# Kernel optimization log

Measured on AMD Instinct MI355X. Metric: run time of the kernel, lower is better.

## Reference

```python
import jax, jax.numpy as jnp
import numpy as np

EMBED_DIM = 512
NUM_HEADS = 8
HEAD_DIM = EMBED_DIM // NUM_HEADS
B, N, M = 4, 4096, 4096


def setup_inputs() -> dict:
    key = jax.random.key(0)
    ks = jax.random.split(key, 16)
    s = 0.02
    inp = {
        "query": jax.random.normal(ks[0], (B, N, EMBED_DIM), jnp.float32),
        "key": jax.random.normal(ks[1], (B, M, EMBED_DIM), jnp.float32),
        "value": jax.random.normal(ks[2], (B, M, EMBED_DIM), jnp.float32),
        # Linear weights stored as (in, out) so y = x @ W + b (== torch x @ W.T + b)
        "Wq": jax.random.normal(ks[3], (EMBED_DIM, EMBED_DIM), jnp.float32) * s,
        "bq": jnp.zeros((EMBED_DIM,), jnp.float32),
        "Wk": jax.random.normal(ks[4], (EMBED_DIM, EMBED_DIM), jnp.float32) * s,
        "bk": jnp.zeros((EMBED_DIM,), jnp.float32),
        "Wv": jax.random.normal(ks[5], (EMBED_DIM, EMBED_DIM), jnp.float32) * s,
        "bv": jnp.zeros((EMBED_DIM,), jnp.float32),
        # rank expansion MLP acts per-head on head_dim
        "W1": jax.random.normal(ks[6], (HEAD_DIM, HEAD_DIM * 2), jnp.float32) * s,
        "b1": jnp.zeros((HEAD_DIM * 2,), jnp.float32),
        "W2": jax.random.normal(ks[7], (HEAD_DIM * 2, HEAD_DIM), jnp.float32) * s,
        "b2": jnp.zeros((HEAD_DIM,), jnp.float32),
        "Wo": jax.random.normal(ks[8], (EMBED_DIM, EMBED_DIM), jnp.float32) * s,
        "bo": jnp.zeros((EMBED_DIM,), jnp.float32),
    }
    return inp


def reference(query, key, value, Wq, bq, Wk, bk, Wv, bv, W1, b1, W2, b2, Wo, bo):
    b, n, _ = query.shape
    m = key.shape[1]
    H, D = NUM_HEADS, HEAD_DIM
    # ELU+1 feature maps on projected q, k
    q = jax.nn.elu(query @ Wq + bq) + 1.0           # [B,N,E]
    k = jax.nn.elu(key @ Wk + bk) + 1.0             # [B,M,E]
    v = value @ Wv + bv                              # [B,M,E]
    q = q.reshape(b, n, H, D)
    k = k.reshape(b, m, H, D)
    v = v.reshape(b, m, H, D)
    # rank expansion MLP on keys (per head_dim), exact GELU as nn.GELU default
    k_aug = jax.nn.gelu(k @ W1 + b1, approximate=False) @ W2 + b2
    k_aug = jax.nn.elu(k_aug) + 1.0                  # [B,M,H,D]
    # inputs already fp32 (torch .float() casts are identity here)
    k_scaled = k_aug / m                             # normalize over context len
    kv_context = jnp.einsum('bmhd,bmhe->bhde', k_scaled, v)   # [B,H,D,D]
    out = jnp.einsum('bnhd,bhde->bnhe', q, kv_context)        # [B,N,H,D]
    k_sum = k_scaled.sum(axis=1)                      # [B,H,D]
    denom = jnp.einsum('bnhd,bhd->bnh', q, k_sum)     # [B,N,H]
    out = out / jnp.clip(denom, 1e-6, None)[..., None]
    out = jnp.clip(jnp.nan_to_num(out, nan=0.0, posinf=65000.0, neginf=-65000.0),
                   -65000.0, 65000.0)
    out = out.reshape(b, n, H * D)
    return out @ Wo + bo
```

## Files before the change

kernel.cpp:

```cpp
#include <hip/hip_runtime.h>
#include <hip/hip_bf16.h>
#include <cmath>

#define DEV __device__ __forceinline__

typedef __bf16 bf16x8 __attribute__((ext_vector_type(8)));
typedef float f32x4 __attribute__((ext_vector_type(4)));
typedef unsigned int u32;
typedef unsigned short u16;

#define S_VMCNT(N) asm volatile("s_waitcnt vmcnt(" #N ")" ::: "memory")
#define S_LGKM0    asm volatile("s_waitcnt lgkmcnt(0)" ::: "memory")
#define S_FENCE    asm volatile("" ::: "memory")
#define S_BAR      __builtin_amdgcn_s_barrier()

DEV u16 f2bf(float f) {
  union { float f; u32 u; } v;
  v.f = f;
  u32 u = v.u;
  u += 0x7fffu + ((u >> 16) & 1u);
  return (u16)(u >> 16);
}
DEV u32 pk2(float a, float b) {
  union { __hip_bfloat162 h2; u32 u; } v;
  v.h2 = __float22bfloat162_rn(float2{a, b});
  return v.u;
}

DEV void async16(const void* g, void* l) {
  __builtin_amdgcn_global_load_lds((const __attribute__((address_space(1))) u32*)g,
                                   (__attribute__((address_space(3))) u32*)l, 16, 0, 0);
}

DEV int swz(int row, int kq) { return row * 64 + ((kq * 8) ^ ((row & 7) << 3)); }

__global__ __launch_bounds__(256, 2)
void qkv_gemm(const float* __restrict__ qin, const float* __restrict__ kin,
              const float* __restrict__ vin, const u16* __restrict__ WqP,
              const u16* __restrict__ WkP, const u16* __restrict__ WvP,
              const float* __restrict__ bq, const float* __restrict__ bk,
              const float* __restrict__ bv, u16* __restrict__ qact,
              u16* __restrict__ kact, u16* __restrict__ vT)
{
  __shared__ __align__(16) u16 SB[32768];

  const int z = blockIdx.z;
  const float* Af = z == 0 ? qin : z == 1 ? kin : vin;
  const u16* Bp = z == 0 ? WqP : z == 1 ? WkP : WvP;
  const float* bias = z == 0 ? bq : z == 1 ? bk : bv;

  const int tid = threadIdx.x, wv = tid >> 6, lane = tid & 63;
  const int wr = wv >> 1, wc = wv & 1;
  const int lrow = lane & 15, lq = lane >> 4;
  const long r0 = (long)blockIdx.x * 128;
  const int c0 = blockIdx.y * 128;

  f32x4 acc[4][4] = {};
  float4 rA[2][8];

  auto loadA = [&](float4* dst, int T) {
#pragma unroll
    for (int it = 0; it < 4; ++it) {
      const int s = it * 256 + tid;
      const int row = s >> 3, kq = s & 7;
      const float* g = Af + (r0 + row) * 512 + T * 64 + kq * 8;
      dst[2 * it]     = *(const float4*)g;
      dst[2 * it + 1] = *(const float4*)(g + 4);
    }
  };
  auto cvtStoreA = [&](const float4* src, u16* bufA) {
#pragma unroll
    for (int it = 0; it < 4; ++it) {
      const int s = it * 256 + tid;
      const int row = s >> 3, kq = s & 7;
      union { u32 q[4]; uint4 v; } pk;
      pk.q[0] = pk2(src[2 * it].x, src[2 * it].y);
      pk.q[1] = pk2(src[2 * it].z, src[2 * it].w);
      pk.q[2] = pk2(src[2 * it + 1].x, src[2 * it + 1].y);
      pk.q[3] = pk2(src[2 * it + 1].z, src[2 * it + 1].w);
      *(uint4*)&bufA[swz(row, kq)] = pk.v;
    }
  };
  auto issueB = [&](int T, u16* bufB) {
#pragma unroll
    for (int it = 0; it < 4; ++it) {
      const int sl = it * 256 + wv * 64;
      async16(Bp + ((long)blockIdx.y * 8 + T) * 8192 + (sl + lane) * 8, &bufB[sl * 8]);
    }
  };
  auto computeT = [&](const u16* Ac, const u16* Bc) {
#pragma unroll
    for (int subk = 0; subk < 2; ++subk) {
      bf16x8 af[4], bfr[4];
#pragma unroll
      for (int i = 0; i < 4; ++i)
        af[i] = *(const bf16x8*)&Ac[swz(wr * 64 + i * 16 + lrow, subk * 4 + lq)];
#pragma unroll
      for (int j = 0; j < 4; ++j)
        bfr[j] = *(const bf16x8*)&Bc[swz(wc * 64 + j * 16 + lrow, subk * 4 + lq)];
#pragma unroll
      for (int i = 0; i < 4; ++i)
#pragma unroll
        for (int j = 0; j < 4; ++j)
          acc[i][j] = __builtin_amdgcn_mfma_f32_16x16x32_bf16(af[i], bfr[j], acc[i][j], 0, 0, 0);
    }
  };

  issueB(0, SB + 8192);
  S_FENCE;
  loadA(rA[0], 0);
  loadA(rA[1], 1);
  cvtStoreA(rA[0], SB);
  S_LGKM0;
  S_VMCNT(8);
  S_BAR;

#pragma unroll
  for (int t = 0; t < 8; ++t) {
    const int cur = t & 1, nxt = 1 - cur;
    u16* Ac = SB + cur * 16384;
    u16* Bc = Ac + 8192;
    u16* An = SB + nxt * 16384;
    u16* Bn = An + 8192;
    if (t < 7) issueB(t + 1, Bn);
    S_FENCE;
    if (t < 6) loadA(rA[cur], t + 2);
    if (t < 7) cvtStoreA(rA[nxt], An);
    computeT(Ac, Bc);
    S_LGKM0;
    if (t < 6)       { S_VMCNT(8); }
    else if (t == 6) { S_VMCNT(0); }
    S_BAR;
  }

  if (z < 2) {
    u16* Y = z == 0 ? qact : kact;
#pragma unroll
    for (int i = 0; i < 4; ++i) {
#pragma unroll
      for (int j = 0; j < 4; ++j) {
        const int col = c0 + wc * 64 + j * 16 + lrow;
        const float bvv = bias[col];
#pragma unroll
        for (int p = 0; p < 4; ++p) {
          float o = acc[i][j][p] + bvv;
          o = (o > 0.f) ? (o + 1.f) : __expf(o);
          const long row = r0 + wr * 64 + i * 16 + lq * 4 + p;
          Y[row * 512 + col] = f2bf(o);
        }
      }
    }
  } else {
    u16* LTv = SB + wv * 4608;
#pragma unroll
    for (int i = 0; i < 4; ++i) {
#pragma unroll
      for (int j = 0; j < 4; ++j) {
        const int col = c0 + wc * 64 + j * 16 + lrow;
        const float bvv = bias[col];
        ushort4 w;
        w.x = f2bf(acc[i][j][0] + bvv);
        w.y = f2bf(acc[i][j][1] + bvv);
        w.z = f2bf(acc[i][j][2] + bvv);
        w.w = f2bf(acc[i][j][3] + bvv);
        *(ushort4*)&LTv[(j * 16 + lrow) * 72 + i * 16 + lq * 4] = w;
      }
    }
    const int b = (int)(r0 >> 12);
    const int h = (c0 + wc * 64) >> 6;
    const int mg0 = (int)(r0 & 4095) + wr * 64;
#pragma unroll
    for (int ps = 0; ps < 8; ++ps) {
      const int e = ps * 8 + (lane >> 3);
      const int mq = (lane & 7) * 8;
      uint4 v = *(const uint4*)&LTv[e * 72 + mq];
      *(uint4*)(vT + (((long)b * 8 + h) * 64 + e) * 4096 + mg0 + mq) = v;
    }
  }
}

__global__ __launch_bounds__(256, 2)
void out_gemm(const u16* __restrict__ A, const u16* __restrict__ Bt,
              const float* __restrict__ bias, float* __restrict__ Y)
{
  __shared__ __align__(16) u16 SB[32768];
  const int tid = threadIdx.x, wv = tid >> 6, lane = tid & 63;
  const int wr = wv >> 1, wc = wv & 1;
  const int lrow = lane & 15, lq = lane >> 4;
  const long r0 = (long)blockIdx.x * 128;
  const int c0 = blockIdx.y * 128;

  auto stage = [&](int T, u16* buf) {
#pragma unroll
    for (int it = 0; it < 4; ++it) {
      const int sl = it * 256 + wv * 64;
      async16(A  + ((long)blockIdx.x * 8 + T) * 8192 + (sl + lane) * 8, &buf[sl * 8]);
      async16(Bt + ((long)blockIdx.y * 8 + T) * 8192 + (sl + lane) * 8, &buf[8192 + sl * 8]);
    }
  };

  f32x4 acc[4][4] = {};
  stage(0, SB);
  S_VMCNT(0);
  S_BAR;

#pragma unroll
  for (int t = 0; t < 8; ++t) {
    const int cur = t & 1, nxt = 1 - cur;
    if (t < 7) stage(t + 1, SB + nxt * 16384);
    const u16* Ac = SB + cur * 16384;
    const u16* Bc = Ac + 8192;
#pragma unroll
    for (int subk = 0; subk < 2; ++subk) {
      bf16x8 af[4], bfr[4];
#pragma unroll
      for (int i = 0; i < 4; ++i)
        af[i] = *(const bf16x8*)&Ac[swz(wr * 64 + i * 16 + lrow, subk * 4 + lq)];
#pragma unroll
      for (int j = 0; j < 4; ++j)
        bfr[j] = *(const bf16x8*)&Bc[swz(wc * 64 + j * 16 + lrow, subk * 4 + lq)];
#pragma unroll
      for (int i = 0; i < 4; ++i)
#pragma unroll
        for (int j = 0; j < 4; ++j)
          acc[i][j] = __builtin_amdgcn_mfma_f32_16x16x32_bf16(af[i], bfr[j], acc[i][j], 0, 0, 0);
    }
    S_LGKM0;
    if (t < 7) { S_VMCNT(0); }
    S_BAR;
  }
#pragma unroll
  for (int i = 0; i < 4; ++i) {
#pragma unroll
    for (int j = 0; j < 4; ++j) {
      const int col = c0 + wc * 64 + j * 16 + lrow;
      const float bv = bias[col];
#pragma unroll
      for (int p = 0; p < 4; ++p) {
        const long row = r0 + wr * 64 + i * 16 + lq * 4 + p;
        Y[row * 512 + col] = acc[i][j][p] + bv;
      }
    }
  }
}

struct TArgs {
  const float* src[6];
  u16* dst[6];
  int K[6];
  int N[6];
};
__global__ __launch_bounds__(256)
void transpose_w(TArgs a)
{
  const int m = blockIdx.z;
  const int K = a.K[m], N = a.N[m];
  const int kt = blockIdx.y * 64, nt = blockIdx.x * 64;
  if (kt >= K || nt >= N) return;
  const float* src = a.src[m];
  u16* dst = a.dst[m];
  __shared__ u16 t[64][72];
  const int tx = threadIdx.x & 15, ty = threadIdx.x >> 4;
#pragma unroll
  for (int rr = 0; rr < 64; rr += 16) {
    const int k = kt + ty + rr;
    float4 v = *(const float4*)(src + (long)k * N + nt + tx * 4);
    t[tx * 4 + 0][ty + rr] = f2bf(v.x);
    t[tx * 4 + 1][ty + rr] = f2bf(v.y);
    t[tx * 4 + 2][ty + rr] = f2bf(v.z);
    t[tx * 4 + 3][ty + rr] = f2bf(v.w);
  }
  __syncthreads();
  if (m < 4) {
    const int ktile = kt >> 6;
#pragma unroll
    for (int it = 0; it < 2; ++it) {
      const int s = threadIdx.x + it * 256;
      const int r = s >> 3, c = (s & 7) * 8;
      const int n = nt + r;
      const int colblk = n >> 7, cl = n & 127;
      ushort4 u0 = *(ushort4*)&t[r][c];
      ushort4 u1 = *(ushort4*)&t[r][c + 4];
      u16* d = dst + ((long)colblk * 8 + ktile) * 8192 + cl * 64 + (c ^ ((cl & 7) << 3));
      *(ushort4*)d = u0;
      *(ushort4*)(d + 4) = u1;
    }
  } else {
#pragma unroll
    for (int it = 0; it < 2; ++it) {
      const int s = threadIdx.x + it * 256;
      const int r = s >> 3, c = (s & 7) * 8;
      ushort4 u0 = *(ushort4*)&t[r][c];
      ushort4 u1 = *(ushort4*)&t[r][c + 4];
      *(ushort4*)(dst + (long)(nt + r) * K + kt + c) = u0;
      *(ushort4*)(dst + (long)(nt + r) * K + kt + c + 4) = u1;
    }
  }
}

__global__ __launch_bounds__(256)
void mlp_fused(const u16* __restrict__ kact, const u16* __restrict__ W1T,
               const u16* __restrict__ W2T, const float* __restrict__ b1,
               const float* __restrict__ b2, u16* __restrict__ kaT, float invM)
{
  __shared__ __align__(16) u16 SB[27136];
  u16* As  = SB;
  u16* W1p = SB + 9216;
  u16* W2p = SB + 18432;
  u16* hid = SB;
  u16* LT2 = SB;

  const int tid = threadIdx.x, wv = tid >> 6, lane = tid & 63;
  const int lrow = lane & 15, lq = lane >> 4;
  const int bh = blockIdx.y, b = bh >> 3, h = bh & 7;
  const int m0 = blockIdx.x * 128;
  const long kbase = ((long)b * 4096 + m0) * 512 + h * 64;

#pragma unroll
  for (int i = 0; i < 4; ++i) {
    const int c = i * 256 + tid;
    const int row = c >> 3, p = c & 7;
    uint4 v = *(const uint4*)(kact + kbase + (long)row * 512 + p * 8);
    *(uint4*)&As[row * 72 + p * 8] = v;
  }
#pragma unroll
  for (int i = 0; i < 4; ++i) {
    const int c = i * 256 + tid;
    const int row = c >> 3, p = c & 7;
    uint4 v = *(const uint4*)(W1T + c * 8);
    *(uint4*)&W1p[row * 72 + p * 8] = v;
  }
#pragma unroll
  for (int i = 0; i < 4; ++i) {
    const int c = i * 256 + tid;
    const int row = c >> 4, p = c & 15;
    uint4 v = *(const uint4*)(W2T + c * 8);
    *(uint4*)&W2p[row * 136 + p * 8] = v;
  }
  __syncthreads();

  const int c0 = (wv >> 1) * 64, mh0 = (wv & 1) * 64;
  f32x4 acc1[4][4] = {};
#pragma unroll
  for (int kt = 0; kt < 2; ++kt) {
    bf16x8 wa[4], kb[4];
#pragma unroll
    for (int i = 0; i < 4; ++i)
      wa[i] = *(const bf16x8*)&W1p[(c0 + i * 16 + lrow) * 72 + kt * 32 + lq * 8];
#pragma unroll
    for (int j = 0; j < 4; ++j)
      kb[j] = *(const bf16x8*)&As[(mh0 + j * 16 + lrow) * 72 + kt * 32 + lq * 8];
#pragma unroll
    for (int i = 0; i < 4; ++i)
#pragma unroll
      for (int j = 0; j < 4; ++j)
        acc1[i][j] = __builtin_amdgcn_mfma_f32_16x16x32_bf16(wa[i], kb[j], acc1[i][j], 0, 0, 0);
  }
  __syncthreads();

#pragma unroll
  for (int i = 0; i < 4; ++i) {
    const int cc = c0 + i * 16 + lq * 4;
    float4 bv = *(const float4*)(b1 + cc);
#pragma unroll
    for (int j = 0; j < 4; ++j) {
      const int m = mh0 + j * 16 + lrow;
      float x0 = acc1[i][j][0] + bv.x, x1 = acc1[i][j][1] + bv.y;
      float x2 = acc1[i][j][2] + bv.z, x3 = acc1[i][j][3] + bv.w;
      ushort4 w;
      w.x = f2bf(0.5f * x0 * (1.f + erff(x0 * 0.7071067811865475f)));
      w.y = f2bf(0.5f * x1 * (1.f + erff(x1 * 0.7071067811865475f)));
      w.z = f2bf(0.5f * x2 * (1.f + erff(x2 * 0.7071067811865475f)));
      w.w = f2bf(0.5f * x3 * (1.f + erff(x3 * 0.7071067811865475f)));
      *(ushort4*)&hid[m * 136 + cc] = w;
    }
  }
  __syncthreads();

  const int d0 = (wv >> 1) * 32, mh2 = (wv & 1) * 64;
  f32x4 acc2[4][2] = {};
#pragma unroll
  for (int kt = 0; kt < 4; ++kt) {
    bf16x8 wa[2], hb[4];
#pragma unroll
    for (int i = 0; i < 2; ++i)
      wa[i] = *(const bf16x8*)&W2p[(d0 + i * 16 + lrow) * 136 + kt * 32 + lq * 8];
#pragma unroll
    for (int j = 0; j < 4; ++j)
      hb[j] = *(const bf16x8*)&hid[(mh2 + j * 16 + lrow) * 136 + kt * 32 + lq * 8];
#pragma unroll
    for (int j = 0; j < 4; ++j)
#pragma unroll
      for (int i = 0; i < 2; ++i)
        acc2[j][i] = __builtin_amdgcn_mfma_f32_16x16x32_bf16(hb[j], wa[i], acc2[j][i], 0, 0, 0);
  }
  __syncthreads();

#pragma unroll
  for (int i = 0; i < 2; ++i) {
    const int d = d0 + i * 16 + lrow;
    const float bd = b2[d];
#pragma unroll
    for (int j = 0; j < 4; ++j) {
      const int ml = mh2 + j * 16 + lq * 4;
      ushort4 w;
#pragma unroll
      for (int p = 0; p < 4; ++p) {
        float v = acc2[j][i][p] + bd;
        v = ((v > 0.f) ? (v + 1.f) : __expf(v)) * invM;
        ((u16*)&w)[p] = f2bf(v);
      }
      *(ushort4*)&LT2[d * 136 + ml] = w;
    }
  }
  __syncthreads();
#pragma unroll
  for (int it = 0; it < 4; ++it) {
    const int c = it * 256 + tid;
    const int d = c >> 4, mq = (c & 15) * 8;
    uint4 v = *(const uint4*)&LT2[d * 136 + mq];
    *(uint4*)(kaT + ((long)bh * 64 + d) * 4096 + m0 + mq) = v;
  }
}

__global__ __launch_bounds__(256, 2)
void kv_gemm(const u16* __restrict__ kaT, const u16* __restrict__ vT,
             float* __restrict__ kvp, float* __restrict__ ksp)
{
  const int sp = blockIdx.x;
  const int bh = blockIdx.y;
  __shared__ __align__(16) u16 SB[32768];
  const int tid = threadIdx.x, wv = tid >> 6, lane = tid & 63;
  const int lrow = lane & 15, lq = lane >> 4;
  f32x4 acc[4][4] = {};
  f32x4 accs[4] = {};
  bf16x8 ones;
#pragma unroll
  for (int z = 0; z < 8; ++z) ones[z] = (__bf16)1.0f;
  const long base = (long)bh * 64 * 4096;

#pragma unroll
  for (int ph = 0; ph < 2; ++ph) {
    const int m0 = sp * 256 + ph * 128;
#pragma unroll
    for (int i = 0; i < 4; ++i) {
      const int s = (wv * 4 + i) * 64 + lane;
      const int chunk = s >> 8, row = (s >> 2) & 63, part = s & 3;
      const long g = base + (long)row * 4096 + m0 + chunk * 32 + part * 8;
      async16(kaT + g, &SB[ph * 16384 + (wv * 4 + i) * 512]);
      async16(vT + g, &SB[ph * 16384 + 8192 + (wv * 4 + i) * 512]);
    }
    S_FENCE;
  }

#pragma unroll
  for (int ph = 0; ph < 2; ++ph) {
    if (ph == 0) { S_VMCNT(8); } else { S_VMCNT(0); }
    const u16* As = SB + ph * 16384;
    const u16* Bs = As + 8192;
    bf16x8 af[4], bfr[4];
#pragma unroll
    for (int i = 0; i < 4; ++i)
      af[i] = *(const bf16x8*)&As[wv * 2048 + (i * 16 + lrow) * 32 + lq * 8];
#pragma unroll
    for (int j = 0; j < 4; ++j)
      bfr[j] = *(const bf16x8*)&Bs[wv * 2048 + (j * 16 + lrow) * 32 + lq * 8];
#pragma unroll
    for (int i = 0; i < 4; ++i) {
#pragma unroll
      for (int j = 0; j < 4; ++j)
        acc[i][j] = __builtin_amdgcn_mfma_f32_16x16x32_bf16(af[i], bfr[j], acc[i][j], 0, 0, 0);
      accs[i] = __builtin_amdgcn_mfma_f32_16x16x32_bf16(af[i], ones, accs[i], 0, 0, 0);
    }
  }

  float* red = (float*)SB;
  float* ksr = red + 64 * 68;
  for (int w = 0; w < 4; ++w) {
    __syncthreads();
    if (wv == w) {
#pragma unroll
      for (int i = 0; i < 4; ++i) {
#pragma unroll
        for (int j = 0; j < 4; ++j) {
          const int e = j * 16 + lrow, dd = i * 16 + lq * 4;
          float* p = &red[e * 68 + dd];
          if (w == 0) { p[0] = acc[i][j][0]; p[1] = acc[i][j][1]; p[2] = acc[i][j][2]; p[3] = acc[i][j][3]; }
          else        { p[0] += acc[i][j][0]; p[1] += acc[i][j][1]; p[2] += acc[i][j][2]; p[3] += acc[i][j][3]; }
        }
        if (lrow == 0) {
          const int dd = i * 16 + lq * 4;
#pragma unroll
          for (int p2 = 0; p2 < 4; ++p2) {
            if (w == 0) ksr[dd + p2] = accs[i][p2];
            else        ksr[dd + p2] += accs[i][p2];
          }
        }
      }
    }
  }
  __syncthreads();
  float* kvo = kvp + ((long)sp * 32 + bh) * 4096;
  for (int s = tid; s < 4096; s += 256) kvo[s] = red[(s >> 6) * 68 + (s & 63)];
  if (tid < 64) ksp[(sp * 32 + bh) * 64 + tid] = ksr[tid];
}

__global__ __launch_bounds__(256)
void kv_reduce(const float* __restrict__ kvp, const float* __restrict__ ksp,
               u16* __restrict__ kvT, u16* __restrict__ ksumT)
{
  const int bh = blockIdx.x;
  const int t = threadIdx.x;
  const int s0 = blockIdx.y * 512;
#pragma unroll
  for (int i = 0; i < 2; ++i) {
    const int s = s0 + i * 256 + t;
    float v = 0.f;
#pragma unroll
    for (int sp = 0; sp < 16; ++sp) v += kvp[((long)sp * 32 + bh) * 4096 + s];
    kvT[(long)bh * 4096 + s] = f2bf(v);
  }
  if (blockIdx.y == 0 && t < 64) {
    float v = 0.f;
#pragma unroll
    for (int sp = 0; sp < 16; ++sp) v += ksp[(sp * 32 + bh) * 64 + t];
    ksumT[bh * 64 + t] = f2bf(v);
  }
}

__global__ __launch_bounds__(256)
void attn_mfma(const u16* __restrict__ q, const u16* __restrict__ kvT,
               const u16* __restrict__ ksumT, u16* __restrict__ attn)
{
  __shared__ u16 SB[17408];
  const int tid = threadIdx.x, wv = tid >> 6, lane = tid & 63;
  const int lrow = lane & 15, lq = lane >> 4;
  const int n0 = blockIdx.x * 256;
  const int bh = blockIdx.y, b = bh >> 3, h = bh & 7;
  u16* As = SB;

#pragma unroll
  for (int half = 0; half < 2; ++half)
#pragma unroll
    for (int i = 0; i < 4; ++i) {
      const int s = (wv * 4 + i) * 64 + lane;
      async16(q + ((long)(b * 4096 + n0 + (s >> 2))) * 512 + h * 64 + half * 32 + (s & 3) * 8,
              &As[half * 8192 + (wv * 4 + i) * 512]);
    }
  bf16x8 bfr[2][4], ks[2];
#pragma unroll
  for (int half = 0; half < 2; ++half) {
#pragma unroll
    for (int j = 0; j < 4; ++j)
      bfr[half][j] = *(const bf16x8*)(kvT + ((long)bh * 64 + j * 16 + lrow) * 64 + half * 32 + lq * 8);
    ks[half] = *(const bf16x8*)(ksumT + bh * 64 + half * 32 + lq * 8);
  }
  __syncthreads();

  f32x4 acc[4][4] = {};
  f32x4 accd[4] = {};
#pragma unroll
  for (int half = 0; half < 2; ++half) {
    bf16x8 af[4];
#pragma unroll
    for (int i = 0; i < 4; ++i)
      af[i] = *(const bf16x8*)&As[half * 8192 + (wv * 64 + i * 16 + lrow) * 32 + lq * 8];
#pragma unroll
    for (int i = 0; i < 4; ++i) {
#pragma unroll
      for (int j = 0; j < 4; ++j)
        acc[i][j] = __builtin_amdgcn_mfma_f32_16x16x32_bf16(af[i], bfr[half][j], acc[i][j], 0, 0, 0);
      accd[i] = __builtin_amdgcn_mfma_f32_16x16x32_bf16(af[i], ks[half], accd[i], 0, 0, 0);
    }
  }
  __syncthreads();

  u16* LT = SB;
#pragma unroll
  for (int i = 0; i < 4; ++i) {
    float dinv[4];
#pragma unroll
    for (int p = 0; p < 4; ++p) dinv[p] = 1.f / fmaxf(accd[i][p], 1e-6f);
#pragma unroll
    for (int j = 0; j < 4; ++j) {
      const int e = j * 16 + lrow;
      const int nl0 = i * 16 + lq * 4;
      ushort4 w;
      float x0 = acc[i][j][0] * dinv[0], x1 = acc[i][j][1] * dinv[1];
      float x2 = acc[i][j][2] * dinv[2], x3 = acc[i][j][3] * dinv[3];
      if (!(x0 == x0)) x0 = 0.f;
      if (!(x1 == x1)) x1 = 0.f;
      if (!(x2 == x2)) x2 = 0.f;
      if (!(x3 == x3)) x3 = 0.f;
      w.x = f2bf(fminf(65000.f, fmaxf(-65000.f, x0)));
      w.y = f2bf(fminf(65000.f, fmaxf(-65000.f, x1)));
      w.z = f2bf(fminf(65000.f, fmaxf(-65000.f, x2)));
      w.w = f2bf(fminf(65000.f, fmaxf(-65000.f, x3)));
      *(ushort4*)&LT[wv * 4352 + e * 68 + nl0] = w;
    }
  }
  __syncthreads();
#pragma unroll
  for (int it = 0; it < 8; ++it) {
    const int c = it * 256 + tid;
    const int n = c & 255, ec = c >> 8;
    const int wr2 = n >> 6, nl = n & 63;
    ushort4 w0, w1;
    w0.x = LT[wr2 * 4352 + (ec * 8 + 0) * 68 + nl];
    w0.y = LT[wr2 * 4352 + (ec * 8 + 1) * 68 + nl];
    w0.z = LT[wr2 * 4352 + (ec * 8 + 2) * 68 + nl];
    w0.w = LT[wr2 * 4352 + (ec * 8 + 3) * 68 + nl];
    w1.x = LT[wr2 * 4352 + (ec * 8 + 4) * 68 + nl];
    w1.y = LT[wr2 * 4352 + (ec * 8 + 5) * 68 + nl];
    w1.z = LT[wr2 * 4352 + (ec * 8 + 6) * 68 + nl];
    w1.w = LT[wr2 * 4352 + (ec * 8 + 7) * 68 + nl];
    const int ng = b * 4096 + n0 + n;
    const int rowblk = ng >> 7, rl = ng & 127;
    u16* dst = attn + ((long)rowblk * 8 + h) * 8192 + rl * 64 + ((ec * 8) ^ ((rl & 7) << 3));
    *(ushort4*)dst = w0;
    *(ushort4*)(dst + 4) = w1;
  }
}

static constexpr long U = 8388608;

extern "C" void kernel_launch(void* const* d_in, const int* in_sizes, int n_in,
                              void* d_out, int out_size, void* d_ws, size_t ws_size,
                              hipStream_t stream)
{
  const float* query = (const float*)d_in[0];
  const float* key   = (const float*)d_in[1];
  const float* value = (const float*)d_in[2];
  const float* Wq = (const float*)d_in[3];
  const float* bq = (const float*)d_in[4];
  const float* Wk = (const float*)d_in[5];
  const float* bk = (const float*)d_in[6];
  const float* Wv = (const float*)d_in[7];
  const float* bv = (const float*)d_in[8];
  const float* W1 = (const float*)d_in[9];
  const float* b1 = (const float*)d_in[10];
  const float* W2 = (const float*)d_in[11];
  const float* b2 = (const float*)d_in[12];
  const float* Wo = (const float*)d_in[13];
  const float* bo = (const float*)d_in[14];

  u16* wsh = (u16*)d_ws;
  u16* qact = wsh;
  u16* kact = wsh + U;
  u16* vT   = wsh + 2 * U;
  u16* kaT  = wsh + 3 * U;
  u16* attn = wsh + 4 * U;

  float* fp  = (float*)(wsh + 5 * U);
  float* kvp = fp;
  float* ksp = fp + 2097152;
  u16* kvTg   = (u16*)(fp + 2129920);
  u16* ksumTg = kvTg + 131072;
  u16* wtb = ksumTg + 2048;
  u16* WqT = wtb;
  u16* WkT = wtb + 262144;
  u16* WvT = wtb + 524288;
  u16* WoT = wtb + 786432;
  u16* W1T = wtb + 1048576;
  u16* W2T = wtb + 1056768;

  dim3 blk(256);
  const float invM = 1.f / 4096.f;

  TArgs ta;
  ta.src[0] = Wq; ta.dst[0] = WqT; ta.K[0] = 512; ta.N[0] = 512;
  ta.src[1] = Wk; ta.dst[1] = WkT; ta.K[1] = 512; ta.N[1] = 512;
  ta.src[2] = Wv; ta.dst[2] = WvT; ta.K[2] = 512; ta.N[2] = 512;
  ta.src[3] = Wo; ta.dst[3] = WoT; ta.K[3] = 512; ta.N[3] = 512;
  ta.src[4] = W1; ta.dst[4] = W1T; ta.K[4] = 64;  ta.N[4] = 128;
  ta.src[5] = W2; ta.dst[5] = W2T; ta.K[5] = 128; ta.N[5] = 64;
  transpose_w<<<dim3(8, 8, 6), blk, 0, stream>>>(ta);

  qkv_gemm<<<dim3(128, 4, 3), blk, 0, stream>>>(query, key, value, WqT, WkT, WvT,
                                                bq, bk, bv, qact, kact, vT);
  mlp_fused<<<dim3(32, 32), blk, 0, stream>>>(kact, W1T, W2T, b1, b2, kaT, invM);
  kv_gemm<<<dim3(16, 32), blk, 0, stream>>>(kaT, vT, kvp, ksp);
  kv_reduce<<<dim3(32, 8), blk, 0, stream>>>(kvp, ksp, kvTg, ksumTg);
  attn_mfma<<<dim3(16, 32), blk, 0, stream>>>(qact, kvTg, ksumTg, attn);
  out_gemm<<<dim3(128, 4), blk, 0, stream>>>(attn, WoT, bo, (float*)d_out);
}
```

Before: 256.1 us.

## Fuse key rank-expansion MLP into QKV GEMM epilogue, dropping kact round-trip

The key-projection blocks of the QKV GEMM now run the per-head MLP (W1, GELU, W2, ELU+1, scale) directly on their accumulators via shared memory. Each block covers two heads and loops over them. This removes the separate mlp_fused launch and the bf16 kact write and read through global memory. In exchange, the z=1 blocks get a much longer epilogue with extra barriers and weight reloads per head, which may leave those blocks imbalanced against the q and v blocks and raise register pressure.

After: 251.7 us. Within noise of the previous version (-1.7%).

```diff
diff --git a/kernel.cpp b/kernel.cpp
--- a/kernel.cpp
+++ b/kernel.cpp
@@ -39,8 +39,10 @@
               const float* __restrict__ vin, const u16* __restrict__ WqP,
               const u16* __restrict__ WkP, const u16* __restrict__ WvP,
               const float* __restrict__ bq, const float* __restrict__ bk,
-              const float* __restrict__ bv, u16* __restrict__ qact,
-              u16* __restrict__ kact, u16* __restrict__ vT)
+              const float* __restrict__ bv, const u16* __restrict__ W1T,
+              const u16* __restrict__ W2T, const float* __restrict__ b1,
+              const float* __restrict__ b2, u16* __restrict__ qact,
+              u16* __restrict__ vT, u16* __restrict__ kaT, float invM)
 {
   __shared__ __align__(16) u16 SB[32768];
 
@@ -133,8 +135,7 @@
     S_BAR;
   }
 
-  if (z < 2) {
-    u16* Y = z == 0 ? qact : kact;
+  if (z == 0) {
 #pragma unroll
     for (int i = 0; i < 4; ++i) {
 #pragma unroll
@@ -146,11 +147,12 @@
           float o = acc[i][j][p] + bvv;
           o = (o > 0.f) ? (o + 1.f) : __expf(o);
           const long row = r0 + wr * 64 + i * 16 + lq * 4 + p;
-          Y[row * 512 + col] = f2bf(o);
+          qact[row * 512 + col] = f2bf(o);
         }
       }
     }
-  } else {
+  } else if (z == 2) {
+    __syncthreads();
     u16* LTv = SB + wv * 4608;
 #pragma unroll
     for (int i = 0; i < 4; ++i) {
@@ -169,12 +171,140 @@
     const int b = (int)(r0 >> 12);
     const int h = (c0 + wc * 64) >> 6;
     const int mg0 = (int)(r0 & 4095) + wr * 64;
+    __syncthreads();
 #pragma unroll
     for (int ps = 0; ps < 8; ++ps) {
       const int e = ps * 8 + (lane >> 3);
       const int mq = (lane & 7) * 8;
       uint4 v = *(const uint4*)&LTv[e * 72 + mq];
       *(uint4*)(vT + (((long)b * 8 + h) * 64 + e) * 4096 + mg0 + mq) = v;
+    }
+  } else {
+    u16* As_k = SB;
+    u16* W1p  = SB + 9216;
+    u16* W2p  = SB + 18432;
+    u16* hid  = SB;
+    u16* LT2  = SB;
+    const int b   = (int)(r0 >> 12);
+    const int m0g = (int)(r0 & 4095);
+    const int h0  = c0 >> 6;
+    __syncthreads();
+
+    for (int hh = 0; hh < 2; ++hh) {
+#pragma unroll
+      for (int i = 0; i < 4; ++i) {
+        const int c = i * 256 + tid;
+        *(uint4*)&W1p[(c >> 3) * 72 + (c & 7) * 8] = *(const uint4*)(W1T + c * 8);
+      }
+#pragma unroll
+      for (int i = 0; i < 4; ++i) {
+        const int c = i * 256 + tid;
+        *(uint4*)&W2p[(c >> 4) * 136 + (c & 15) * 8] = *(const uint4*)(W2T + c * 8);
+      }
+      if (wc == hh) {
+#pragma unroll
+        for (int i = 0; i < 4; ++i)
+#pragma unroll
+          for (int j = 0; j < 4; ++j) {
+            const int col = c0 + wc * 64 + j * 16 + lrow;
+            const float bvv = bias[col];
+            const int d = j * 16 + lrow;
+            const int mb = wr * 64 + i * 16 + lq * 4;
+#pragma unroll
+            for (int p = 0; p < 4; ++p) {
+              float o = acc[i][j][p] + bvv;
+              o = (o > 0.f) ? (o + 1.f) : __expf(o);
+              As_k[(mb + p) * 72 + d] = f2bf(o);
+            }
+          }
+      }
+      __syncthreads();
+
+      const int c0m = (wv >> 1) * 64, mh0 = (wv & 1) * 64;
+      f32x4 acc1[4][4] = {};
+#pragma unroll
+      for (int kt = 0; kt < 2; ++kt) {
+        bf16x8 wa[4], kb[4];
+#pragma unroll
+        for (int i = 0; i < 4; ++i)
+          wa[i] = *(const bf16x8*)&W1p[(c0m + i * 16 + lrow) * 72 + kt * 32 + lq * 8];
+#pragma unroll
+        for (int j = 0; j < 4; ++j)
+          kb[j] = *(const bf16x8*)&As_k[(mh0 + j * 16 + lrow) * 72 + kt * 32 + lq * 8];
+#pragma unroll
+        for (int i = 0; i < 4; ++i)
+#pragma unroll
+          for (int j = 0; j < 4; ++j)
+            acc1[i][j] = __builtin_amdgcn_mfma_f32_16x16x32_bf16(wa[i], kb[j], acc1[i][j], 0, 0, 0);
+      }
+      __syncthreads();
+
+#pragma unroll
+      for (int i = 0; i < 4; ++i) {
+        const int cc = c0m + i * 16 + lq * 4;
+        float4 bv4 = *(const float4*)(b1 + cc);
+#pragma unroll
+        for (int j = 0; j < 4; ++j) {
+          const int m = mh0 + j * 16 + lrow;
+          float x0 = acc1[i][j][0] + bv4.x, x1 = acc1[i][j][1] + bv4.y;
+          float x2 = acc1[i][j][2] + bv4.z, x3 = acc1[i][j][3] + bv4.w;
+          ushort4 w;
+          w.x = f2bf(0.5f * x0 * (1.f + erff(x0 * 0.7071067811865475f)));
+          w.y = f2bf(0.5f * x1 * (1.f + erff(x1 * 0.7071067811865475f)));
+          w.z = f2bf(0.5f * x2 * (1.f + erff(x2 * 0.7071067811865475f)));
+          w.w = f2bf(0.5f * x3 * (1.f + erff(x3 * 0.7071067811865475f)));
+          *(ushort4*)&hid[m * 136 + cc] = w;
+        }
+      }
+      __syncthreads();
+
+      const int d0 = (wv >> 1) * 32, mh2 = (wv & 1) * 64;
+      f32x4 acc2[4][2] = {};
+#pragma unroll
+      for (int kt = 0; kt < 4; ++kt) {
+        bf16x8 wa2[2], hb[4];
+#pragma unroll
+        for (int i = 0; i < 2; ++i)
+          wa2[i] = *(const bf16x8*)&W2p[(d0 + i * 16 + lrow) * 136 + kt * 32 + lq * 8];
+#pragma unroll
+        for (int j = 0; j < 4; ++j)
+          hb[j] = *(const bf16x8*)&hid[(mh2 + j * 16 + lrow) * 136 + kt * 32 + lq * 8];
+#pragma unroll
+        for (int j = 0; j < 4; ++j)
+#pragma unroll
+          for (int i = 0; i < 2; ++i)
+            acc2[j][i] = __builtin_amdgcn_mfma_f32_16x16x32_bf16(hb[j], wa2[i], acc2[j][i], 0, 0, 0);
+      }
+      __syncthreads();
+
+#pragma unroll
+      for (int i = 0; i < 2; ++i) {
+        const int d = d0 + i * 16 + lrow;
+        const float bd = b2[d];
+#pragma unroll
+        for (int j = 0; j < 4; ++j) {
+          const int ml = mh2 + j * 16 + lq * 4;
+          ushort4 w;
+#pragma unroll
+          for (int p = 0; p < 4; ++p) {
+            float v = acc2[j][i][p] + bd;
+            v = ((v > 0.f) ? (v + 1.f) : __expf(v)) * invM;
+            ((u16*)&w)[p] = f2bf(v);
+          }
+          *(ushort4*)&LT2[d * 136 + ml] = w;
+        }
+      }
+      __syncthreads();
+
+      const int bh2 = b * 8 + h0 + hh;
+#pragma unroll
+      for (int it = 0; it < 4; ++it) {
+        const int c = it * 256 + tid;
+        const int d = c >> 4, mq = (c & 15) * 8;
+        uint4 v = *(const uint4*)&LT2[d * 136 + mq];
+        *(uint4*)(kaT + ((long)bh2 * 64 + d) * 4096 + m0g + mq) = v;
+      }
+      __syncthreads();
     }
   }
 }
@@ -295,131 +425,6 @@
       *(ushort4*)(dst + (long)(nt + r) * K + kt + c) = u0;
       *(ushort4*)(dst + (long)(nt + r) * K + kt + c + 4) = u1;
     }
-  }
-}
-
-__global__ __launch_bounds__(256)
-void mlp_fused(const u16* __restrict__ kact, const u16* __restrict__ W1T,
-               const u16* __restrict__ W2T, const float* __restrict__ b1,
-               const float* __restrict__ b2, u16* __restrict__ kaT, float invM)
-{
-  __shared__ __align__(16) u16 SB[27136];
-  u16* As  = SB;
-  u16* W1p = SB + 9216;
-  u16* W2p = SB + 18432;
-  u16* hid = SB;
-  u16* LT2 = SB;
-
-  const int tid = threadIdx.x, wv = tid >> 6, lane = tid & 63;
-  const int lrow = lane & 15, lq = lane >> 4;
-  const int bh = blockIdx.y, b = bh >> 3, h = bh & 7;
-  const int m0 = blockIdx.x * 128;
-  const long kbase = ((long)b * 4096 + m0) * 512 + h * 64;
-
-#pragma unroll
-  for (int i = 0; i < 4; ++i) {
-    const int c = i * 256 + tid;
-    const int row = c >> 3, p = c & 7;
-    uint4 v = *(const uint4*)(kact + kbase + (long)row * 512 + p * 8);
-    *(uint4*)&As[row * 72 + p * 8] = v;
-  }
-#pragma unroll
-  for (int i = 0; i < 4; ++i) {
-    const int c = i * 256 + tid;
-    const int row = c >> 3, p = c & 7;
-    uint4 v = *(const uint4*)(W1T + c * 8);
-    *(uint4*)&W1p[row * 72 + p * 8] = v;
-  }
-#pragma unroll
-  for (int i = 0; i < 4; ++i) {
-    const int c = i * 256 + tid;
-    const int row = c >> 4, p = c & 15;
-    uint4 v = *(const uint4*)(W2T + c * 8);
-    *(uint4*)&W2p[row * 136 + p * 8] = v;
-  }
-  __syncthreads();
-
-  const int c0 = (wv >> 1) * 64, mh0 = (wv & 1) * 64;
-  f32x4 acc1[4][4] = {};
-#pragma unroll
-  for (int kt = 0; kt < 2; ++kt) {
-    bf16x8 wa[4], kb[4];
-#pragma unroll
-    for (int i = 0; i < 4; ++i)
-      wa[i] = *(const bf16x8*)&W1p[(c0 + i * 16 + lrow) * 72 + kt * 32 + lq * 8];
-#pragma unroll
-    for (int j = 0; j < 4; ++j)
-      kb[j] = *(const bf16x8*)&As[(mh0 + j * 16 + lrow) * 72 + kt * 32 + lq * 8];
-#pragma unroll
-    for (int i = 0; i < 4; ++i)
-#pragma unroll
-      for (int j = 0; j < 4; ++j)
-        acc1[i][j] = __builtin_amdgcn_mfma_f32_16x16x32_bf16(wa[i], kb[j], acc1[i][j], 0, 0, 0);
-  }
-  __syncthreads();
-
-#pragma unroll
-  for (int i = 0; i < 4; ++i) {
-    const int cc = c0 + i * 16 + lq * 4;
-    float4 bv = *(const float4*)(b1 + cc);
-#pragma unroll
-    for (int j = 0; j < 4; ++j) {
-      const int m = mh0 + j * 16 + lrow;
-      float x0 = acc1[i][j][0] + bv.x, x1 = acc1[i][j][1] + bv.y;
-      float x2 = acc1[i][j][2] + bv.z, x3 = acc1[i][j][3] + bv.w;
-      ushort4 w;
-      w.x = f2bf(0.5f * x0 * (1.f + erff(x0 * 0.7071067811865475f)));
-      w.y = f2bf(0.5f * x1 * (1.f + erff(x1 * 0.7071067811865475f)));
-      w.z = f2bf(0.5f * x2 * (1.f + erff(x2 * 0.7071067811865475f)));
-      w.w = f2bf(0.5f * x3 * (1.f + erff(x3 * 0.7071067811865475f)));
-      *(ushort4*)&hid[m * 136 + cc] = w;
-    }
-  }
-  __syncthreads();
-
-  const int d0 = (wv >> 1) * 32, mh2 = (wv & 1) * 64;
-  f32x4 acc2[4][2] = {};
-#pragma unroll
-  for (int kt = 0; kt < 4; ++kt) {
-    bf16x8 wa[2], hb[4];
-#pragma unroll
-    for (int i = 0; i < 2; ++i)
-      wa[i] = *(const bf16x8*)&W2p[(d0 + i * 16 + lrow) * 136 + kt * 32 + lq * 8];
-#pragma unroll
-    for (int j = 0; j < 4; ++j)
-      hb[j] = *(const bf16x8*)&hid[(mh2 + j * 16 + lrow) * 136 + kt * 32 + lq * 8];
-#pragma unroll
-    for (int j = 0; j < 4; ++j)
-#pragma unroll
-      for (int i = 0; i < 2; ++i)
-        acc2[j][i] = __builtin_amdgcn_mfma_f32_16x16x32_bf16(hb[j], wa[i], acc2[j][i], 0, 0, 0);
-  }
-  __syncthreads();
-
-#pragma unroll
-  for (int i = 0; i < 2; ++i) {
-    const int d = d0 + i * 16 + lrow;
-    const float bd = b2[d];
-#pragma unroll
-    for (int j = 0; j < 4; ++j) {
-      const int ml = mh2 + j * 16 + lq * 4;
-      ushort4 w;
-#pragma unroll
-      for (int p = 0; p < 4; ++p) {
-        float v = acc2[j][i][p] + bd;
-        v = ((v > 0.f) ? (v + 1.f) : __expf(v)) * invM;
-        ((u16*)&w)[p] = f2bf(v);
-      }
-      *(ushort4*)&LT2[d * 136 + ml] = w;
-    }
-  }
-  __syncthreads();
-#pragma unroll
-  for (int it = 0; it < 4; ++it) {
-    const int c = it * 256 + tid;
-    const int d = c >> 4, mq = (c & 15) * 8;
-    uint4 v = *(const uint4*)&LT2[d * 136 + mq];
-    *(uint4*)(kaT + ((long)bh * 64 + d) * 4096 + m0 + mq) = v;
   }
 }
 
@@ -646,7 +651,6 @@
 
   u16* wsh = (u16*)d_ws;
   u16* qact = wsh;
-  u16* kact = wsh + U;
   u16* vT   = wsh + 2 * U;
   u16* kaT  = wsh + 3 * U;
   u16* attn = wsh + 4 * U;
@@ -677,8 +681,8 @@
   transpose_w<<<dim3(8, 8, 6), blk, 0, stream>>>(ta);
 
   qkv_gemm<<<dim3(128, 4, 3), blk, 0, stream>>>(query, key, value, WqT, WkT, WvT,
-                                                bq, bk, bv, qact, kact, vT);
-  mlp_fused<<<dim3(32, 32), blk, 0, stream>>>(kact, W1T, W2T, b1, b2, kaT, invM);
+                                                bq, bk, bv, W1T, W2T, b1, b2,
+                                                qact, vT, kaT, invM);
   kv_gemm<<<dim3(16, 32), blk, 0, stream>>>(kaT, vT, kvp, ksp);
   kv_reduce<<<dim3(32, 8), blk, 0, stream>>>(kvp, ksp, kvTg, ksumTg);
   attn_mfma<<<dim3(16, 32), blk, 0, stream>>>(qact, kvTg, ksumTg, attn);
```
